# Optimization experiments

Measured on AMD Instinct MI355X. Metric: run time of the kernel, lower is better.

## Reference

```python
import jax, jax.numpy as jnp
import numpy as np

B, T, D, H = 64, 2048, 256, 256

def setup_inputs() -> dict:
    key = jax.random.key(0)
    k_x, k_z, k_r, k_h = jax.random.split(key, 4)
    gate_in = D + H
    # lecun_normal: std = 1/sqrt(fan_in)
    s = 1.0 / np.sqrt(gate_in)
    return {
        "x": jax.random.normal(k_x, (B, T, D), dtype=jnp.float32),
        "W_z": jax.random.normal(k_z, (gate_in, H), dtype=jnp.float32) * s,
        "b_z": jnp.zeros((H,), dtype=jnp.float32),
        "W_r": jax.random.normal(k_r, (gate_in, H), dtype=jnp.float32) * s,
        "b_r": jnp.zeros((H,), dtype=jnp.float32),
        "W_h": jax.random.normal(k_h, (gate_in, H), dtype=jnp.float32) * s,
        "b_h": jnp.zeros((H,), dtype=jnp.float32),
    }

def reference(x, W_z, b_z, W_r, b_r, W_h, b_h):
    Bx, Tx, Dx = x.shape
    Hx = W_z.shape[1]

    def scan_fn(h_prev, x_t):
        xh = jnp.concatenate([x_t, h_prev], axis=-1)        # [B, D+H]
        z = jax.nn.sigmoid(xh @ W_z + b_z)                   # [B, H]
        r = jax.nn.sigmoid(xh @ W_r + b_r)                   # [B, H]
        xrh = jnp.concatenate([x_t, r * h_prev], axis=-1)   # [B, D+H]
        h_hat = jnp.tanh(xrh @ W_h + b_h)                    # [B, H]
        h_new = (1 - z) * h_prev + z * h_hat
        return h_new, h_new

    h0 = jnp.zeros((Bx, Hx), dtype=x.dtype)
    x_t = jnp.transpose(x, (1, 0, 2))                        # [T, B, D]
    _, all_h = jax.lax.scan(scan_fn, h0, x_t)                # [T, B, H]
    return jnp.transpose(all_h, (1, 0, 2))                   # [B, T, H]
```

## Files before the change

kernel.cpp:

```cpp
#include <hip/hip_runtime.h>

typedef _Float16 half2_t __attribute__((ext_vector_type(2)));

#define NB 64
#define NT 2048
#define ND 256
#define NH 256
#define NTHR 256
#define CHUNK 32
#define NCHUNK (NT / CHUNK)

#define XT_STRIDE 132
#define LDS_DW (32 * XT_STRIDE + 16)

__device__ __forceinline__ float sigmoid_f(float x) { return 1.f / (1.f + __expf(-x)); }
__device__ __forceinline__ float tanh_f(float x)    { return 1.f - 2.f / (1.f + __expf(2.f * x)); }
__device__ __forceinline__ half2_t mkh2(float a, float b) {
    half2_t r; r.x = (_Float16)a; r.y = (_Float16)b; return r;
}
__device__ __forceinline__ half2_t u2h2(unsigned u) { return __builtin_bit_cast(half2_t, u); }
__device__ __forceinline__ float h2get(unsigned u, int idx) {
    half2_t h = u2h2(u);
    return idx ? (float)h.y : (float)h.x;
}
__device__ __forceinline__ int dot4i8(int a, int b, int c) {
#if __has_builtin(__builtin_amdgcn_sdot4)
    return __builtin_amdgcn_sdot4(a, b, c, false);
#else
    int d;
    asm("v_dot4_i32_i8 %0, %1, %2, %3" : "=v"(d) : "v"(a), "v"(b), "v"(c));
    return d;
#endif
}
#define BAR_LDS() asm volatile("s_waitcnt lgkmcnt(0)\n\ts_barrier" ::: "memory")

extern "C" __global__ void __launch_bounds__(NTHR)
gru_fused(const float* __restrict__ x,
          const float* __restrict__ Wz, const float* __restrict__ bz,
          const float* __restrict__ Wr, const float* __restrict__ br,
          const float* __restrict__ Wh, const float* __restrict__ bh,
          float* __restrict__ out,
          unsigned* prodflag, unsigned* consflag,
          unsigned long long* preZR, unsigned* preH, int ring)
{
    __shared__ __align__(16) unsigned smem[LDS_DW];
    const int tid = threadIdx.x;
    const int bid = blockIdx.x;
    const int rmask = ring - 1;

    if (bid >= NB) {
        const int pb = bid - NB;
        const int g  = pb >> 6;
        const int b  = pb & 63;
        const float* W    = (g == 0) ? Wz : (g == 1) ? Wr : Wh;
        const float* bias = (g == 0) ? bz : (g == 1) ? br : bh;
        const int kh = tid & 1;
        const int c2 = tid >> 1;
        const int c0 = c2 * 2, c1 = c0 + 1;

        half2_t wa[64], wb[64];
        #pragma unroll
        for (int j = 0; j < 64; ++j) {
            const int k = kh * 128 + 2 * j;
            wa[j] = mkh2(W[k * NH + c0], W[(k + 1) * NH + c0]);
            wb[j] = mkh2(W[k * NH + c1], W[(k + 1) * NH + c1]);
        }
        const float bv0 = bias[c0], bv1 = bias[c1];

        for (int ch = 0; ch < NCHUNK; ++ch) {
            const int lead = ch * CHUNK + CHUNK - ring;
            if (lead > 0) {
                if (tid == 0) {
                    unsigned it = 0;
                    while ((int)__hip_atomic_load(&consflag[b], __ATOMIC_RELAXED,
                                                  __HIP_MEMORY_SCOPE_AGENT) < lead) {
                        __builtin_amdgcn_s_sleep(8);
                        if (++it > (1u << 20)) break;
                    }
                }
                __syncthreads();
            }
            const int t0 = ch * CHUNK;
            {
                const float4* xs = reinterpret_cast<const float4*>(
                    x + (size_t)b * NT * ND + (size_t)t0 * ND);
                #pragma unroll
                for (int rep = 0; rep < 8; ++rep) {
                    const int f = rep * NTHR + tid;
                    const float4 v = xs[f];
                    const int tt = f >> 6;
                    const int u2 = f & 63;
                    uint2 pk;
                    pk.x = __builtin_bit_cast(unsigned, mkh2(v.x, v.y));
                    pk.y = __builtin_bit_cast(unsigned, mkh2(v.z, v.w));
                    *reinterpret_cast<uint2*>(&smem[tt * XT_STRIDE + u2 * 2]) = pk;
                }
            }
            __syncthreads();
            #pragma unroll 1
            for (int t = 0; t < CHUNK; ++t) {
                const uint4* xr4 = reinterpret_cast<const uint4*>(
                    &smem[t * XT_STRIDE + kh * 64]);
                float a00 = 0.f, a01 = 0.f, a10 = 0.f, a11 = 0.f;
                #pragma unroll
                for (int i = 0; i < 16; ++i) {
                    const uint4 xv = xr4[i];
                    a00 = __builtin_amdgcn_fdot2(u2h2(xv.x), wa[i*4+0], a00, false);
                    a01 = __builtin_amdgcn_fdot2(u2h2(xv.y), wa[i*4+1], a01, false);
                    a00 = __builtin_amdgcn_fdot2(u2h2(xv.z), wa[i*4+2], a00, false);
                    a01 = __builtin_amdgcn_fdot2(u2h2(xv.w), wa[i*4+3], a01, false);
                    a10 = __builtin_amdgcn_fdot2(u2h2(xv.x), wb[i*4+0], a10, false);
                    a11 = __builtin_amdgcn_fdot2(u2h2(xv.y), wb[i*4+1], a11, false);
                    a10 = __builtin_amdgcn_fdot2(u2h2(xv.z), wb[i*4+2], a10, false);
                    a11 = __builtin_amdgcn_fdot2(u2h2(xv.w), wb[i*4+3], a11, false);
                }
                float a0 = a00 + a01, a1 = a10 + a11;
                a0 += __shfl_xor(a0, 1, 64);
                a1 += __shfl_xor(a1, 1, 64);
                a0 += bv0; a1 += bv1;
                if (kh == 0) {
                    const unsigned pk = __builtin_bit_cast(unsigned, mkh2(a0, a1));
                    const size_t slot = (size_t)b * ring + ((t0 + t) & rmask);
                    if (g == 2) {
                        __hip_atomic_store(&preH[slot * 128 + c2], pk,
                                           __ATOMIC_RELAXED, __HIP_MEMORY_SCOPE_AGENT);
                    } else {
                        unsigned* zr32 = reinterpret_cast<unsigned*>(&preZR[slot * 128 + c2]);
                        __hip_atomic_store(&zr32[g], pk,
                                           __ATOMIC_RELAXED, __HIP_MEMORY_SCOPE_AGENT);
                    }
                }
            }
            asm volatile("s_waitcnt vmcnt(0)" ::: "memory");
            __syncthreads();
            if (tid == 0)
                __hip_atomic_store(&prodflag[b * 3 + g], (unsigned)(ch + 1),
                                   __ATOMIC_RELAXED, __HIP_MEMORY_SCOPE_AGENT);
            __syncthreads();
        }
        return;
    }

    const int b    = bid;
    const int c    = tid;
    const int lane = tid & 63;
    const int sub  = c & 1;

    float mxz = 1e-8f, mxr = 1e-8f, mxh = 1e-8f;
    #pragma unroll 4
    for (int j = 0; j < 256; ++j) {
        mxz = fmaxf(mxz, fabsf(Wz[(ND + j) * NH + c]));
        mxr = fmaxf(mxr, fabsf(Wr[(ND + j) * NH + c]));
        mxh = fmaxf(mxh, fabsf(Wh[(ND + j) * NH + c]));
    }
    const float qsz = 127.0f / mxz, qsr = 127.0f / mxr, qsh = 127.0f / mxh;
    const float deqz = mxz / (127.0f * 127.0f);
    const float deqr = mxr / (127.0f * 127.0f);
    const float deqh = mxh / (127.0f * 127.0f);

    uint4 wz4[16], wr4[16], wh4[16];
    #pragma unroll
    for (int i = 0; i < 16; ++i) {
        unsigned dz[4], dr[4], dh[4];
        #pragma unroll
        for (int d = 0; d < 4; ++d) {
            unsigned az = 0, ar = 0, ah = 0;
            #pragma unroll
            for (int j = 0; j < 4; ++j) {
                const int k = ND + (i * 4 + d) * 4 + j;
                const int qz = __float2int_rn(Wz[k * NH + c] * qsz);
                const int qr = __float2int_rn(Wr[k * NH + c] * qsr);
                const int qh = __float2int_rn(Wh[k * NH + c] * qsh);
                az |= ((unsigned)(qz & 255)) << (8 * j);
                ar |= ((unsigned)(qr & 255)) << (8 * j);
                ah |= ((unsigned)(qh & 255)) << (8 * j);
            }
            dz[d] = az; dr[d] = ar; dh[d] = ah;
        }
        wz4[i] = make_uint4(dz[0], dz[1], dz[2], dz[3]);
        wr4[i] = make_uint4(dr[0], dr[1], dr[2], dr[3]);
        wh4[i] = make_uint4(dh[0], dh[1], dh[2], dh[3]);
    }

    if (tid < 128) smem[tid] = 0u;
    float hreg = 0.f;

    if (tid < 3) {
        unsigned it = 0;
        while (__hip_atomic_load(&prodflag[b * 3 + tid], __ATOMIC_RELAXED,
                                 __HIP_MEMORY_SCOPE_AGENT) < 1u) {
            __builtin_amdgcn_s_sleep(8);
            if (++it > (1u << 20)) break;
        }
    }
    __syncthreads();

    const unsigned long long* zrb = preZR + (size_t)b * ring * 128 + (c >> 1);
    const unsigned*           hhb = preH  + (size_t)b * ring * 128 + (c >> 1);
    float* outb = out + (size_t)b * NT * NH + c;
    const uint4* lds4 = reinterpret_cast<const uint4*>(smem);
    char* ldsb = reinterpret_cast<char*>(smem);

    unsigned long long zr_c = __hip_atomic_load(zrb, __ATOMIC_RELAXED, __HIP_MEMORY_SCOPE_AGENT);
    unsigned           hh_c = __hip_atomic_load(hhb, __ATOMIC_RELAXED, __HIP_MEMORY_SCOPE_AGENT);

    #pragma unroll 1
    for (int t = 0; t < NT; ++t) {
        const int tn = t + 1;
        const bool pf = (tn < NT) && ((tn & (CHUNK - 1)) != 0);
        unsigned long long zr_n = 0; unsigned hh_n = 0;
        if (pf) {
            const int so = (tn & rmask) * 128;
            zr_n = __hip_atomic_load(zrb + so, __ATOMIC_RELAXED, __HIP_MEMORY_SCOPE_AGENT);
            hh_n = __hip_atomic_load(hhb + so, __ATOMIC_RELAXED, __HIP_MEMORY_SCOPE_AGENT);
        }

        const uint4 hvec = lds4[lane & 15];
        int az0 = 0, az1 = 0, az2 = 0, az3 = 0;
        int ar0 = 0, ar1 = 0, ar2 = 0, ar3 = 0;
        #pragma unroll
        for (int i = 0; i < 16; ++i) {
            const int sx = __builtin_amdgcn_readlane((int)hvec.x, i);
            const int sy = __builtin_amdgcn_readlane((int)hvec.y, i);
            const int sz = __builtin_amdgcn_readlane((int)hvec.z, i);
            const int sw = __builtin_amdgcn_readlane((int)hvec.w, i);
            az0 = dot4i8(sx, (int)wz4[i].x, az0);
            az1 = dot4i8(sy, (int)wz4[i].y, az1);
            az2 = dot4i8(sz, (int)wz4[i].z, az2);
            az3 = dot4i8(sw, (int)wz4[i].w, az3);
            ar0 = dot4i8(sx, (int)wr4[i].x, ar0);
            ar1 = dot4i8(sy, (int)wr4[i].y, ar1);
            ar2 = dot4i8(sz, (int)wr4[i].z, ar2);
            ar3 = dot4i8(sw, (int)wr4[i].w, ar3);
        }
        const float azf = (float)((az0 + az1) + (az2 + az3)) * deqz;
        const float arf = (float)((ar0 + ar1) + (ar2 + ar3)) * deqr;
        const float z = sigmoid_f(azf + h2get((unsigned)(zr_c & 0xffffffffu), sub));
        const float r = sigmoid_f(arf + h2get((unsigned)(zr_c >> 32), sub));
        const float v = r * hreg;
        ldsb[256 + c] = (char)__float2int_rn(v * 127.0f);
        BAR_LDS();

        const uint4 vvec = lds4[16 + (lane & 15)];
        int ah0 = 0, ah1 = 0, ah2 = 0, ah3 = 0;
        #pragma unroll
        for (int i = 0; i < 16; ++i) {
            const int sx = __builtin_amdgcn_readlane((int)vvec.x, i);
            const int sy = __builtin_amdgcn_readlane((int)vvec.y, i);
            const int sz = __builtin_amdgcn_readlane((int)vvec.z, i);
            const int sw = __builtin_amdgcn_readlane((int)vvec.w, i);
            ah0 = dot4i8(sx, (int)wh4[i].x, ah0);
            ah1 = dot4i8(sy, (int)wh4[i].y, ah1);
            ah2 = dot4i8(sz, (int)wh4[i].z, ah2);
            ah3 = dot4i8(sw, (int)wh4[i].w, ah3);
        }
        const float ahf = (float)((ah0 + ah1) + (ah2 + ah3)) * deqh;
        const float hhat = tanh_f(ahf + h2get(hh_c, sub));
        const float hn = hreg + z * (hhat - hreg);
        hreg = hn;
        outb[(size_t)t * NH] = hn;
        ldsb[c] = (char)__float2int_rn(hn * 127.0f);
        BAR_LDS();

        if (pf) {
            zr_c = zr_n; hh_c = hh_n;
        } else if (tn < NT) {
            if (tid == 0)
                __hip_atomic_store(&consflag[b], (unsigned)tn,
                                   __ATOMIC_RELAXED, __HIP_MEMORY_SCOPE_AGENT);
            const unsigned need = (unsigned)((tn >> 5) + 1);
            if (tid < 3) {
                unsigned it = 0;
                while (__hip_atomic_load(&prodflag[b * 3 + tid], __ATOMIC_RELAXED,
                                         __HIP_MEMORY_SCOPE_AGENT) < need) {
                    __builtin_amdgcn_s_sleep(8);
                    if (++it > (1u << 20)) break;
                }
            }
            __syncthreads();
            const int so = (tn & rmask) * 128;
            zr_c = __hip_atomic_load(zrb + so, __ATOMIC_RELAXED, __HIP_MEMORY_SCOPE_AGENT);
            hh_c = __hip_atomic_load(hhb + so, __ATOMIC_RELAXED, __HIP_MEMORY_SCOPE_AGENT);
        }
    }
}

extern "C" void kernel_launch(void* const* d_in, const int* in_sizes, int n_in,
                              void* d_out, int out_size, void* d_ws, size_t ws_size,
                              hipStream_t stream) {
    const float* x  = (const float*)d_in[0];
    const float* Wz = (const float*)d_in[1];
    const float* bz = (const float*)d_in[2];
    const float* Wr = (const float*)d_in[3];
    const float* br = (const float*)d_in[4];
    const float* Wh = (const float*)d_in[5];
    const float* bh = (const float*)d_in[6];
    float* outp = (float*)d_out;

    const size_t base = 4096;
    int ring = 32;
    for (int r = 2048; r >= 32; r >>= 1) {
        const size_t need = base + (size_t)NB * r * 128 * 12;
        if (need <= ws_size) { ring = r; break; }
    }
    char* w = (char*)d_ws;
    unsigned* prodflag = (unsigned*)w;
    unsigned* consflag = (unsigned*)(w + 1024);
    unsigned long long* preZR = (unsigned long long*)(w + base);
    unsigned* preH = (unsigned*)(w + base + (size_t)NB * ring * 128 * 8);

    hipMemsetAsync(w, 0, 4096, stream);
    gru_fused<<<256, NTHR, 0, stream>>>(x, Wz, bz, Wr, br, Wh, bh, outp,
                                        prodflag, consflag, preZR, preH, ring);
}
```

Before: 2.063 ms.

## Process two batch rows per consumer block to share register-resident weights

Each consumer block now runs the recurrence for two batch elements at once, halving consumer blocks from 64 to 32. The int8 weight registers are reused for both rows, giving twice the independent dot4 chains per wavefront to hide latency, and barriers are amortised over two rows. The prefetch of the next step's precomputed gates is also moved to after the first gate stage, just before the mid-step barrier. The cost is roughly double the serial work per timestep on each block, so the critical path per step lengthens unless latency hiding compensates.

```diff
diff --git a/kernel.cpp b/kernel.cpp
--- a/kernel.cpp
+++ b/kernel.cpp
@@ -7,6 +7,8 @@
 #define ND 256
 #define NH 256
 #define NTHR 256
+#define NCONS 32
+#define GRID (NCONS + 192)
 #define CHUNK 32
 #define NCHUNK (NT / CHUNK)
 
@@ -48,8 +50,8 @@
     const int bid = blockIdx.x;
     const int rmask = ring - 1;
 
-    if (bid >= NB) {
-        const int pb = bid - NB;
+    if (bid >= NCONS) {
+        const int pb = bid - NCONS;
         const int g  = pb >> 6;
         const int b  = pb & 63;
         const float* W    = (g == 0) ? Wz : (g == 1) ? Wr : Wh;
@@ -141,7 +143,8 @@
         return;
     }
 
-    const int b    = bid;
+    const int b0   = bid * 2;
+    const int b1   = b0 + 1;
     const int c    = tid;
     const int lane = tid & 63;
     const int sub  = c & 1;
@@ -182,12 +185,14 @@
         wh4[i] = make_uint4(dh[0], dh[1], dh[2], dh[3]);
     }
 
-    if (tid < 128) smem[tid] = 0u;
-    float hreg = 0.f;
-
-    if (tid < 3) {
+    smem[tid] = 0u;
+    float hreg0 = 0.f, hreg1 = 0.f;
+
+    if (tid < 6) {
+        const int bb = (tid < 3) ? b0 : b1;
+        const int g  = (tid < 3) ? tid : tid - 3;
         unsigned it = 0;
-        while (__hip_atomic_load(&prodflag[b * 3 + tid], __ATOMIC_RELAXED,
+        while (__hip_atomic_load(&prodflag[bb * 3 + g], __ATOMIC_RELAXED,
                                  __HIP_MEMORY_SCOPE_AGENT) < 1u) {
             __builtin_amdgcn_s_sleep(8);
             if (++it > (1u << 20)) break;
@@ -195,83 +200,132 @@
     }
     __syncthreads();
 
-    const unsigned long long* zrb = preZR + (size_t)b * ring * 128 + (c >> 1);
-    const unsigned*           hhb = preH  + (size_t)b * ring * 128 + (c >> 1);
-    float* outb = out + (size_t)b * NT * NH + c;
+    const unsigned long long* zrb0 = preZR + (size_t)b0 * ring * 128 + (c >> 1);
+    const unsigned*           hhb0 = preH  + (size_t)b0 * ring * 128 + (c >> 1);
+    const unsigned long long* zrb1 = preZR + (size_t)b1 * ring * 128 + (c >> 1);
+    const unsigned*           hhb1 = preH  + (size_t)b1 * ring * 128 + (c >> 1);
+    float* outb0 = out + (size_t)b0 * NT * NH + c;
+    float* outb1 = out + (size_t)b1 * NT * NH + c;
     const uint4* lds4 = reinterpret_cast<const uint4*>(smem);
     char* ldsb = reinterpret_cast<char*>(smem);
 
-    unsigned long long zr_c = __hip_atomic_load(zrb, __ATOMIC_RELAXED, __HIP_MEMORY_SCOPE_AGENT);
-    unsigned           hh_c = __hip_atomic_load(hhb, __ATOMIC_RELAXED, __HIP_MEMORY_SCOPE_AGENT);
+    unsigned long long zr0 = __hip_atomic_load(zrb0, __ATOMIC_RELAXED, __HIP_MEMORY_SCOPE_AGENT);
+    unsigned           hh0 = __hip_atomic_load(hhb0, __ATOMIC_RELAXED, __HIP_MEMORY_SCOPE_AGENT);
+    unsigned long long zr1 = __hip_atomic_load(zrb1, __ATOMIC_RELAXED, __HIP_MEMORY_SCOPE_AGENT);
+    unsigned           hh1 = __hip_atomic_load(hhb1, __ATOMIC_RELAXED, __HIP_MEMORY_SCOPE_AGENT);
 
     #pragma unroll 1
     for (int t = 0; t < NT; ++t) {
         const int tn = t + 1;
         const bool pf = (tn < NT) && ((tn & (CHUNK - 1)) != 0);
-        unsigned long long zr_n = 0; unsigned hh_n = 0;
+
+        const uint4 hv0 = lds4[lane & 15];
+        const uint4 hv1 = lds4[32 + (lane & 15)];
+        int az00 = 0, az01 = 0, az02 = 0, az03 = 0;
+        int ar00 = 0, ar01 = 0, ar02 = 0, ar03 = 0;
+        int az10 = 0, az11 = 0, az12 = 0, az13 = 0;
+        int ar10 = 0, ar11 = 0, ar12 = 0, ar13 = 0;
+        #pragma unroll
+        for (int i = 0; i < 16; ++i) {
+            const int s0x = __builtin_amdgcn_readlane((int)hv0.x, i);
+            const int s0y = __builtin_amdgcn_readlane((int)hv0.y, i);
+            const int s0z = __builtin_amdgcn_readlane((int)hv0.z, i);
+            const int s0w = __builtin_amdgcn_readlane((int)hv0.w, i);
+            const int s1x = __builtin_amdgcn_readlane((int)hv1.x, i);
+            const int s1y = __builtin_amdgcn_readlane((int)hv1.y, i);
+            const int s1z = __builtin_amdgcn_readlane((int)hv1.z, i);
+            const int s1w = __builtin_amdgcn_readlane((int)hv1.w, i);
+            az00 = dot4i8(s0x, (int)wz4[i].x, az00);
+            az10 = dot4i8(s1x, (int)wz4[i].x, az10);
+            az01 = dot4i8(s0y, (int)wz4[i].y, az01);
+            az11 = dot4i8(s1y, (int)wz4[i].y, az11);
+            az02 = dot4i8(s0z, (int)wz4[i].z, az02);
+            az12 = dot4i8(s1z, (int)wz4[i].z, az12);
+            az03 = dot4i8(s0w, (int)wz4[i].w, az03);
+            az13 = dot4i8(s1w, (int)wz4[i].w, az13);
+            ar00 = dot4i8(s0x, (int)wr4[i].x, ar00);
+            ar10 = dot4i8(s1x, (int)wr4[i].x, ar10);
+            ar01 = dot4i8(s0y, (int)wr4[i].y, ar01);
+            ar11 = dot4i8(s1y, (int)wr4[i].y, ar11);
+            ar02 = dot4i8(s0z, (int)wr4[i].z, ar02);
+            ar12 = dot4i8(s1z, (int)wr4[i].z, ar12);
+            ar03 = dot4i8(s0w, (int)wr4[i].w, ar03);
+            ar13 = dot4i8(s1w, (int)wr4[i].w, ar13);
+        }
+        const float azf0 = (float)((az00 + az01) + (az02 + az03)) * deqz;
+        const float arf0 = (float)((ar00 + ar01) + (ar02 + ar03)) * deqr;
+        const float azf1 = (float)((az10 + az11) + (az12 + az13)) * deqz;
+        const float arf1 = (float)((ar10 + ar11) + (ar12 + ar13)) * deqr;
+        const float z0 = sigmoid_f(azf0 + h2get((unsigned)(zr0 & 0xffffffffu), sub));
+        const float r0 = sigmoid_f(arf0 + h2get((unsigned)(zr0 >> 32), sub));
+        const float z1 = sigmoid_f(azf1 + h2get((unsigned)(zr1 & 0xffffffffu), sub));
+        const float r1 = sigmoid_f(arf1 + h2get((unsigned)(zr1 >> 32), sub));
+        const float v0 = r0 * hreg0;
+        const float v1 = r1 * hreg1;
+        ldsb[256 + c] = (char)__float2int_rn(v0 * 127.0f);
+        ldsb[768 + c] = (char)__float2int_rn(v1 * 127.0f);
+
+        unsigned long long zrn0 = 0, zrn1 = 0; unsigned hhn0 = 0, hhn1 = 0;
         if (pf) {
             const int so = (tn & rmask) * 128;
-            zr_n = __hip_atomic_load(zrb + so, __ATOMIC_RELAXED, __HIP_MEMORY_SCOPE_AGENT);
-            hh_n = __hip_atomic_load(hhb + so, __ATOMIC_RELAXED, __HIP_MEMORY_SCOPE_AGENT);
-        }
-
-        const uint4 hvec = lds4[lane & 15];
-        int az0 = 0, az1 = 0, az2 = 0, az3 = 0;
-        int ar0 = 0, ar1 = 0, ar2 = 0, ar3 = 0;
+            zrn0 = __hip_atomic_load(zrb0 + so, __ATOMIC_RELAXED, __HIP_MEMORY_SCOPE_AGENT);
+            hhn0 = __hip_atomic_load(hhb0 + so, __ATOMIC_RELAXED, __HIP_MEMORY_SCOPE_AGENT);
+            zrn1 = __hip_atomic_load(zrb1 + so, __ATOMIC_RELAXED, __HIP_MEMORY_SCOPE_AGENT);
+            hhn1 = __hip_atomic_load(hhb1 + so, __ATOMIC_RELAXED, __HIP_MEMORY_SCOPE_AGENT);
+        }
+        BAR_LDS();
+
+        const uint4 vv0 = lds4[16 + (lane & 15)];
+        const uint4 vv1 = lds4[48 + (lane & 15)];
+        int ah00 = 0, ah01 = 0, ah02 = 0, ah03 = 0;
+        int ah10 = 0, ah11 = 0, ah12 = 0, ah13 = 0;
         #pragma unroll
         for (int i = 0; i < 16; ++i) {
-            const int sx = __builtin_amdgcn_readlane((int)hvec.x, i);
-            const int sy = __builtin_amdgcn_readlane((int)hvec.y, i);
-            const int sz = __builtin_amdgcn_readlane((int)hvec.z, i);
-            const int sw = __builtin_amdgcn_readlane((int)hvec.w, i);
-            az0 = dot4i8(sx, (int)wz4[i].x, az0);
-            az1 = dot4i8(sy, (int)wz4[i].y, az1);
-            az2 = dot4i8(sz, (int)wz4[i].z, az2);
-            az3 = dot4i8(sw, (int)wz4[i].w, az3);
-            ar0 = dot4i8(sx, (int)wr4[i].x, ar0);
-            ar1 = dot4i8(sy, (int)wr4[i].y, ar1);
-            ar2 = dot4i8(sz, (int)wr4[i].z, ar2);
-            ar3 = dot4i8(sw, (int)wr4[i].w, ar3);
-        }
-        const float azf = (float)((az0 + az1) + (az2 + az3)) * deqz;
-        const float arf = (float)((ar0 + ar1) + (ar2 + ar3)) * deqr;
-        const float z = sigmoid_f(azf + h2get((unsigned)(zr_c & 0xffffffffu), sub));
-        const float r = sigmoid_f(arf + h2get((unsigned)(zr_c >> 32), sub));
-        const float v = r * hreg;
-        ldsb[256 + c] = (char)__float2int_rn(v * 127.0f);
+            const int s0x = __builtin_amdgcn_readlane((int)vv0.x, i);
+            const int s0y = __builtin_amdgcn_readlane((int)vv0.y, i);
+            const int s0z = __builtin_amdgcn_readlane((int)vv0.z, i);
+            const int s0w = __builtin_amdgcn_readlane((int)vv0.w, i);
+            const int s1x = __builtin_amdgcn_readlane((int)vv1.x, i);
+            const int s1y = __builtin_amdgcn_readlane((int)vv1.y, i);
+            const int s1z = __builtin_amdgcn_readlane((int)vv1.z, i);
+            const int s1w = __builtin_amdgcn_readlane((int)vv1.w, i);
+            ah00 = dot4i8(s0x, (int)wh4[i].x, ah00);
+            ah10 = dot4i8(s1x, (int)wh4[i].x, ah10);
+            ah01 = dot4i8(s0y, (int)wh4[i].y, ah01);
+            ah11 = dot4i8(s1y, (int)wh4[i].y, ah11);
+            ah02 = dot4i8(s0z, (int)wh4[i].z, ah02);
+            ah12 = dot4i8(s1z, (int)wh4[i].z, ah12);
+            ah03 = dot4i8(s0w, (int)wh4[i].w, ah03);
+            ah13 = dot4i8(s1w, (int)wh4[i].w, ah13);
+        }
+        const float ahf0 = (float)((ah00 + ah01) + (ah02 + ah03)) * deqh;
+        const float ahf1 = (float)((ah10 + ah11) + (ah12 + ah13)) * deqh;
+        const float hhat0 = tanh_f(ahf0 + h2get(hh0, sub));
+        const float hhat1 = tanh_f(ahf1 + h2get(hh1, sub));
+        const float hn0 = hreg0 + z0 * (hhat0 - hreg0);
+        const float hn1 = hreg1 + z1 * (hhat1 - hreg1);
+        hreg0 = hn0; hreg1 = hn1;
+        outb0[(size_t)t * NH] = hn0;
+        outb1[(size_t)t * NH] = hn1;
+        ldsb[c]       = (char)__float2int_rn(hn0 * 127.0f);
+        ldsb[512 + c] = (char)__float2int_rn(hn1 * 127.0f);
         BAR_LDS();
 
-        const uint4 vvec = lds4[16 + (lane & 15)];
-        int ah0 = 0, ah1 = 0, ah2 = 0, ah3 = 0;
-        #pragma unroll
-        for (int i = 0; i < 16; ++i) {
-            const int sx = __builtin_amdgcn_readlane((int)vvec.x, i);
-            const int sy = __builtin_amdgcn_readlane((int)vvec.y, i);
-            const int sz = __builtin_amdgcn_readlane((int)vvec.z, i);
-            const int sw = __builtin_amdgcn_readlane((int)vvec.w, i);
-            ah0 = dot4i8(sx, (int)wh4[i].x, ah0);
-            ah1 = dot4i8(sy, (int)wh4[i].y, ah1);
-            ah2 = dot4i8(sz, (int)wh4[i].z, ah2);
-            ah3 = dot4i8(sw, (int)wh4[i].w, ah3);
-        }
-        const float ahf = (float)((ah0 + ah1) + (ah2 + ah3)) * deqh;
-        const float hhat = tanh_f(ahf + h2get(hh_c, sub));
-        const float hn = hreg + z * (hhat - hreg);
-        hreg = hn;
-        outb[(size_t)t * NH] = hn;
-        ldsb[c] = (char)__float2int_rn(hn * 127.0f);
-        BAR_LDS();
-
         if (pf) {
-            zr_c = zr_n; hh_c = hh_n;
+            zr0 = zrn0; hh0 = hhn0; zr1 = zrn1; hh1 = hhn1;
         } else if (tn < NT) {
-            if (tid == 0)
-                __hip_atomic_store(&consflag[b], (unsigned)tn,
+            if (tid == 0) {
+                __hip_atomic_store(&consflag[b0], (unsigned)tn,
                                    __ATOMIC_RELAXED, __HIP_MEMORY_SCOPE_AGENT);
+                __hip_atomic_store(&consflag[b1], (unsigned)tn,
+                                   __ATOMIC_RELAXED, __HIP_MEMORY_SCOPE_AGENT);
+            }
             const unsigned need = (unsigned)((tn >> 5) + 1);
-            if (tid < 3) {
+            if (tid < 6) {
+                const int bb = (tid < 3) ? b0 : b1;
+                const int g  = (tid < 3) ? tid : tid - 3;
                 unsigned it = 0;
-                while (__hip_atomic_load(&prodflag[b * 3 + tid], __ATOMIC_RELAXED,
+                while (__hip_atomic_load(&prodflag[bb * 3 + g], __ATOMIC_RELAXED,
                                          __HIP_MEMORY_SCOPE_AGENT) < need) {
                     __builtin_amdgcn_s_sleep(8);
                     if (++it > (1u << 20)) break;
@@ -279,8 +333,10 @@
             }
             __syncthreads();
             const int so = (tn & rmask) * 128;
-            zr_c = __hip_atomic_load(zrb + so, __ATOMIC_RELAXED, __HIP_MEMORY_SCOPE_AGENT);
-            hh_c = __hip_atomic_load(hhb + so, __ATOMIC_RELAXED, __HIP_MEMORY_SCOPE_AGENT);
+            zr0 = __hip_atomic_load(zrb0 + so, __ATOMIC_RELAXED, __HIP_MEMORY_SCOPE_AGENT);
+            hh0 = __hip_atomic_load(hhb0 + so, __ATOMIC_RELAXED, __HIP_MEMORY_SCOPE_AGENT);
+            zr1 = __hip_atomic_load(zrb1 + so, __ATOMIC_RELAXED, __HIP_MEMORY_SCOPE_AGENT);
+            hh1 = __hip_atomic_load(hhb1 + so, __ATOMIC_RELAXED, __HIP_MEMORY_SCOPE_AGENT);
         }
     }
 }
@@ -310,6 +366,6 @@
     unsigned* preH = (unsigned*)(w + base + (size_t)NB * ring * 128 * 8);
 
     hipMemsetAsync(w, 0, 4096, stream);
-    gru_fused<<<256, NTHR, 0, stream>>>(x, Wz, bz, Wr, br, Wh, bh, outp,
-                                        prodflag, consflag, preZR, preH, ring);
-}
+    gru_fused<<<GRID, NTHR, 0, stream>>>(x, Wz, bz, Wr, br, Wh, bh, outp,
+                                         prodflag, consflag, preZR, preH, ring);
+}
```

Result: slower. 4.123 ms (+99.8%).

## Broadcast quantized state via uniform LDS loads and DPP-packed dword stores

Applied to the files above, without the earlier changes.

The readlane-based broadcast of the int8 hidden and gated vectors is replaced with wave-uniform LDS uint4 loads inside the dot loops. Byte-wise LDS stores are replaced with DPP shuffles that pack four int8 values into one dword, written by every fourth lane. The z sigmoid is moved after the barrier so it can overlap the wait. The ring buffer is capped at 64 slots, which shrinks the workspace footprint but puts more producer/consumer synchronization on the path.

```diff
diff --git a/kernel.cpp b/kernel.cpp
--- a/kernel.cpp
+++ b/kernel.cpp
@@ -12,6 +12,7 @@
 
 #define XT_STRIDE 132
 #define LDS_DW (32 * XT_STRIDE + 16)
+#define VQ_BYTE 256
 
 __device__ __forceinline__ float sigmoid_f(float x) { return 1.f / (1.f + __expf(-x)); }
 __device__ __forceinline__ float tanh_f(float x)    { return 1.f - 2.f / (1.f + __expf(2.f * x)); }
@@ -23,14 +24,20 @@
     half2_t h = u2h2(u);
     return idx ? (float)h.y : (float)h.x;
 }
-__device__ __forceinline__ int dot4i8(int a, int b, int c) {
+__device__ __forceinline__ int dot4i8(unsigned a, unsigned b, int c) {
 #if __has_builtin(__builtin_amdgcn_sdot4)
-    return __builtin_amdgcn_sdot4(a, b, c, false);
+    return __builtin_amdgcn_sdot4((int)a, (int)b, c, false);
 #else
     int d;
     asm("v_dot4_i32_i8 %0, %1, %2, %3" : "=v"(d) : "v"(a), "v"(b), "v"(c));
     return d;
 #endif
+}
+__device__ __forceinline__ unsigned pack4_dpp(int b) {
+    const int t1 = __builtin_amdgcn_mov_dpp(b, 0xB1, 0xF, 0xF, true);
+    const int p  = (b & 0xFF) | ((t1 & 0xFF) << 8);
+    const int t2 = __builtin_amdgcn_mov_dpp(p, 0x4E, 0xF, 0xF, true);
+    return (unsigned)((p & 0xFFFF) | (t2 << 16));
 }
 #define BAR_LDS() asm volatile("s_waitcnt lgkmcnt(0)\n\ts_barrier" ::: "memory")
 
@@ -143,7 +150,8 @@
 
     const int b    = bid;
     const int c    = tid;
-    const int lane = tid & 63;
+    const int l    = tid & 63;
+    const int w    = tid >> 6;
     const int sub  = c & 1;
 
     float mxz = 1e-8f, mxr = 1e-8f, mxh = 1e-8f;
@@ -198,8 +206,8 @@
     const unsigned long long* zrb = preZR + (size_t)b * ring * 128 + (c >> 1);
     const unsigned*           hhb = preH  + (size_t)b * ring * 128 + (c >> 1);
     float* outb = out + (size_t)b * NT * NH + c;
-    const uint4* lds4 = reinterpret_cast<const uint4*>(smem);
-    char* ldsb = reinterpret_cast<char*>(smem);
+    const uint4* hq4 = reinterpret_cast<const uint4*>(smem);
+    const uint4* vq4 = hq4 + 16;
 
     unsigned long long zr_c = __hip_atomic_load(zrb, __ATOMIC_RELAXED, __HIP_MEMORY_SCOPE_AGENT);
     unsigned           hh_c = __hip_atomic_load(hhb, __ATOMIC_RELAXED, __HIP_MEMORY_SCOPE_AGENT);
@@ -215,51 +223,50 @@
             hh_n = __hip_atomic_load(hhb + so, __ATOMIC_RELAXED, __HIP_MEMORY_SCOPE_AGENT);
         }
 
-        const uint4 hvec = lds4[lane & 15];
         int az0 = 0, az1 = 0, az2 = 0, az3 = 0;
         int ar0 = 0, ar1 = 0, ar2 = 0, ar3 = 0;
         #pragma unroll
         for (int i = 0; i < 16; ++i) {
-            const int sx = __builtin_amdgcn_readlane((int)hvec.x, i);
-            const int sy = __builtin_amdgcn_readlane((int)hvec.y, i);
-            const int sz = __builtin_amdgcn_readlane((int)hvec.z, i);
-            const int sw = __builtin_amdgcn_readlane((int)hvec.w, i);
-            az0 = dot4i8(sx, (int)wz4[i].x, az0);
-            az1 = dot4i8(sy, (int)wz4[i].y, az1);
-            az2 = dot4i8(sz, (int)wz4[i].z, az2);
-            az3 = dot4i8(sw, (int)wz4[i].w, az3);
-            ar0 = dot4i8(sx, (int)wr4[i].x, ar0);
-            ar1 = dot4i8(sy, (int)wr4[i].y, ar1);
-            ar2 = dot4i8(sz, (int)wr4[i].z, ar2);
-            ar3 = dot4i8(sw, (int)wr4[i].w, ar3);
-        }
-        const float azf = (float)((az0 + az1) + (az2 + az3)) * deqz;
+            const uint4 hv = hq4[i];
+            az0 = dot4i8(hv.x, wz4[i].x, az0);
+            az1 = dot4i8(hv.y, wz4[i].y, az1);
+            az2 = dot4i8(hv.z, wz4[i].z, az2);
+            az3 = dot4i8(hv.w, wz4[i].w, az3);
+            ar0 = dot4i8(hv.x, wr4[i].x, ar0);
+            ar1 = dot4i8(hv.y, wr4[i].y, ar1);
+            ar2 = dot4i8(hv.z, wr4[i].z, ar2);
+            ar3 = dot4i8(hv.w, wr4[i].w, ar3);
+        }
+        const float azf = (float)((az0 + az1) + (az2 + az3)) * deqz
+                        + h2get((unsigned)(zr_c & 0xffffffffu), sub);
         const float arf = (float)((ar0 + ar1) + (ar2 + ar3)) * deqr;
-        const float z = sigmoid_f(azf + h2get((unsigned)(zr_c & 0xffffffffu), sub));
         const float r = sigmoid_f(arf + h2get((unsigned)(zr_c >> 32), sub));
         const float v = r * hreg;
-        ldsb[256 + c] = (char)__float2int_rn(v * 127.0f);
+        {
+            const unsigned pk = pack4_dpp(__float2int_rn(v * 127.0f) & 255);
+            if (!(l & 3)) smem[(VQ_BYTE >> 2) + (c >> 2)] = pk;
+        }
         BAR_LDS();
 
-        const uint4 vvec = lds4[16 + (lane & 15)];
+        const float z = sigmoid_f(azf);
         int ah0 = 0, ah1 = 0, ah2 = 0, ah3 = 0;
         #pragma unroll
         for (int i = 0; i < 16; ++i) {
-            const int sx = __builtin_amdgcn_readlane((int)vvec.x, i);
-            const int sy = __builtin_amdgcn_readlane((int)vvec.y, i);
-            const int sz = __builtin_amdgcn_readlane((int)vvec.z, i);
-            const int sw = __builtin_amdgcn_readlane((int)vvec.w, i);
-            ah0 = dot4i8(sx, (int)wh4[i].x, ah0);
-            ah1 = dot4i8(sy, (int)wh4[i].y, ah1);
-            ah2 = dot4i8(sz, (int)wh4[i].z, ah2);
-            ah3 = dot4i8(sw, (int)wh4[i].w, ah3);
+            const uint4 vv = vq4[i];
+            ah0 = dot4i8(vv.x, wh4[i].x, ah0);
+            ah1 = dot4i8(vv.y, wh4[i].y, ah1);
+            ah2 = dot4i8(vv.z, wh4[i].z, ah2);
+            ah3 = dot4i8(vv.w, wh4[i].w, ah3);
         }
         const float ahf = (float)((ah0 + ah1) + (ah2 + ah3)) * deqh;
         const float hhat = tanh_f(ahf + h2get(hh_c, sub));
         const float hn = hreg + z * (hhat - hreg);
         hreg = hn;
         outb[(size_t)t * NH] = hn;
-        ldsb[c] = (char)__float2int_rn(hn * 127.0f);
+        {
+            const unsigned pk = pack4_dpp(__float2int_rn(hn * 127.0f) & 255);
+            if (!(l & 3)) smem[c >> 2] = pk;
+        }
         BAR_LDS();
 
         if (pf) {
@@ -299,7 +306,7 @@
 
     const size_t base = 4096;
     int ring = 32;
-    for (int r = 2048; r >= 32; r >>= 1) {
+    for (int r = 64; r >= 32; r >>= 1) {
         const size_t need = base + (size_t)NB * r * 128 * 12;
         if (need <= ws_size) { ring = r; break; }
     }
```

New measurement: 2.590 ms. +25.5%, slower.
